# Kernel optimization log

Measured on AMD Instinct MI355X. Metric: run time of the kernel, lower is better.

The kernel has to match this reference:

```python
import jax, jax.numpy as jnp
import numpy as np

B, N, D_IN = 8, 1369, 768
S, D, ITERS = 7, 256, 3
RES, SIGMA = 37, 5.0
EPS = 1e-8


def _ln(x, g, b):
    m = jnp.mean(x, -1, keepdims=True)
    v = jnp.mean((x - m) ** 2, -1, keepdims=True)
    return (x - m) * jax.lax.rsqrt(v + 1e-5) * g + b


def _abs_grid():
    xs = jnp.linspace(-1.0, 1.0, RES)
    ys = jnp.linspace(-1.0, 1.0, RES)
    gx, gy = jnp.meshgrid(xs, ys, indexing='xy')
    return jnp.stack([gx.reshape(-1), gy.reshape(-1)], axis=-1)  # [N,2]


def setup_inputs() -> dict:
    key = jax.random.key(0)
    ks = jax.random.split(key, 40)
    i = iter(range(40))
    def w(shape, scale=0.02):
        return (jax.random.normal(ks[next(i)], shape, jnp.float32) * scale).astype(jnp.float32)
    def zeros(shape):
        return jnp.zeros(shape, jnp.float32)
    xav = float(np.sqrt(6.0 / (S + D)))
    inp = {
        'inputs': jax.random.normal(ks[next(i)], (B, N, D_IN), jnp.float32),
        'slots_init_p': jax.random.uniform(ks[next(i)], (1, S, D), jnp.float32, -xav, xav),
        'S_s0': w((1, S, 1, 2)),
        'S_p0': w((1, S, 1, 2)),
        'im_ln1_g': jnp.ones((D_IN,), jnp.float32), 'im_ln1_b': zeros((D_IN,)),
        'im_w1': w((D_IN, D_IN)), 'im_b1': zeros((D_IN,)),
        'im_w2': w((D_IN, D)), 'im_b2': zeros((D,)),
        'im_ln2_g': jnp.ones((D,), jnp.float32), 'im_ln2_b': zeros((D,)),
        'Wq': w((D, D)), 'Wk': w((D, D)), 'Wv': w((D, D)),
        'g_w': w((2, D)), 'g_b': zeros((D,)),
        'f_w1': w((D, D)), 'f_b1': zeros((D,)),
        'f_w2': w((D, D)), 'f_b2': zeros((D,)),
        'ln_g': jnp.ones((D,), jnp.float32), 'ln_b': zeros((D,)),
        'gru_wih': w((D, 3 * D)), 'gru_whh': w((D, 3 * D)),
        'gru_bih': zeros((3 * D,)), 'gru_bhh': zeros((3 * D,)),
        'mlp_ln_g': jnp.ones((D,), jnp.float32), 'mlp_ln_b': zeros((D,)),
        'mlp_w1': w((D, 4 * D)), 'mlp_b1': zeros((4 * D,)),
        'mlp_w2': w((4 * D, D)), 'mlp_b2': zeros((D,)),
        'fin_w': w((D, D)), 'fin_b': zeros((D,)),
    }
    return inp


def reference(inputs, slots_init_p, S_s0, S_p0,
              im_ln1_g, im_ln1_b, im_w1, im_b1, im_w2, im_b2, im_ln2_g, im_ln2_b,
              Wq, Wk, Wv, g_w, g_b, f_w1, f_b1, f_w2, f_b2,
              ln_g, ln_b, gru_wih, gru_whh, gru_bih, gru_bhh,
              mlp_ln_g, mlp_ln_b, mlp_w1, mlp_b1, mlp_w2, mlp_b2,
              fin_w, fin_b):
    abs_grid = _abs_grid()                    # [N,2], constant buffer
    ag = abs_grid[None, None]                 # [1,1,N,2]
    scale = D ** (-0.5)

    slots = jnp.broadcast_to(slots_init_p, (B, S, D))
    slots_init = slots

    # initial_mlp: LN -> Linear -> ReLU -> Linear -> LN (dropout-free eval path)
    x = _ln(inputs, im_ln1_g, im_ln1_b)
    x = jax.nn.relu(x @ im_w1 + im_b1)
    x = x @ im_w2 + im_b2
    x = _ln(x, im_ln2_g, im_ln2_b)            # [B,N,D]
    KX = x @ Wk                                # slot-independent part of K(inputs)
    VX = x @ Wv

    S_p = jnp.broadcast_to(S_p0, (B, S, 1, 2))
    S_s = jnp.broadcast_to(S_s0, (B, S, 1, 2))

    def f_mlp(z):
        return jax.nn.relu(z @ f_w1 + f_b1) @ f_w2 + f_b2

    attn = None
    slots_prev = slots
    for t in range(ITERS + 1):
        if t == ITERS - 1:  # query_opt straight-through trick
            slots = jax.lax.stop_gradient(slots) + slots_init - jax.lax.stop_gradient(slots_init)
        slots_prev = slots
        sn = _ln(slots, ln_g, ln_b)
        rel = (ag - S_p) / (S_s * SIGMA)      # [B,S,N,2]
        grel = rel @ g_w + g_b                # [B,S,N,D]
        k = f_mlp(KX[:, None] + grel)         # [B,S,N,D]
        v = f_mlp(VX[:, None] + grel)
        q = sn @ Wq                           # [B,S,D]
        dots = jnp.einsum('bsd,bsnd->bsn', q, k) * scale
        attn = jax.nn.softmax(dots, axis=1) + EPS   # softmax over slots
        attn = attn / jnp.sum(attn, -1, keepdims=True)
        updates = jnp.einsum('bsnd,bsn->bsd', v, attn)
        S_p = jnp.einsum('bsn,nd->bsd', attn, abs_grid)[:, :, None, :]
        S_s = jnp.sqrt(jnp.einsum('bsnd,bsn->bsd', (ag - S_p) ** 2, attn))[:, :, None, :]
        if t != ITERS:
            # GRUCell (torch gate order r,z,n)
            gi = updates @ gru_wih + gru_bih
            gh = slots_prev @ gru_whh + gru_bhh
            i_r, i_z, i_n = jnp.split(gi, 3, axis=-1)
            h_r, h_z, h_n = jnp.split(gh, 3, axis=-1)
            r = jax.nn.sigmoid(i_r + h_r)
            z = jax.nn.sigmoid(i_z + h_z)
            n = jnp.tanh(i_n + r * h_n)
            slots = (1.0 - z) * n + z * slots_prev
            # residual pre-norm MLP (dropout identity in eval)
            m = _ln(slots, mlp_ln_g, mlp_ln_b)
            m = jax.nn.relu(m @ mlp_w1 + mlp_b1) @ mlp_w2 + mlp_b2
            slots = slots + m
    out = slots_prev @ fin_w + fin_b
    return out, attn
```

## Files before the change

kernel.cpp:

```cpp
#include <hip/hip_runtime.h>

constexpr int CB   = 8;
constexpr int CN   = 1369;
constexpr int CDIN = 768;
constexpr int CS   = 7;
constexpr int CD   = 256;
constexpr int CITERS = 3;
constexpr int CRES = 37;
constexpr float CSIGMA = 5.0f;
constexpr int CBS = CB * CS;
constexpr int CBN = CB * CN;
constexpr int CKV = 2 * CD;
constexpr float LNEPS = 1e-5f;
constexpr float ATTN_EPS = 1e-8f;

typedef unsigned short u16;
typedef short bs8 __attribute__((ext_vector_type(8)));
typedef float f4 __attribute__((ext_vector_type(4)));

__device__ __forceinline__ float ag_x(int n) { return -1.f + (float)(n % CRES) * (2.f / 36.f); }
__device__ __forceinline__ float ag_y(int n) { return -1.f + (float)(n / CRES) * (2.f / 36.f); }

__device__ __forceinline__ u16 bf_rne(float f) {
    unsigned u = __float_as_uint(f);
    return (u16)((u + 0x7FFFu + ((u >> 16) & 1u)) >> 16);
}
__device__ __forceinline__ float bf_to_f(u16 h) { return __uint_as_float(((unsigned)h) << 16); }

__device__ __forceinline__ void split2b(float v, u16& h, u16& m) {
    h = bf_rne(v);
    m = bf_rne(v - bf_to_f(h));
}

__device__ __forceinline__ void async16(const u16* g, u16* l) {
    __builtin_amdgcn_global_load_lds(
        (const __attribute__((address_space(1))) unsigned int*)g,
        (__attribute__((address_space(3))) unsigned int*)l, 16, 0, 0);
}

__device__ __forceinline__ float block_reduce_sum(float v, float* sbuf) {
    #pragma unroll
    for (int off = 32; off > 0; off >>= 1) v += __shfl_down(v, off, 64);
    if ((threadIdx.x & 63) == 0) sbuf[threadIdx.x >> 6] = v;
    __syncthreads();
    if (threadIdx.x == 0) sbuf[0] = sbuf[0] + sbuf[1] + sbuf[2] + sbuf[3];
    __syncthreads();
    float r = sbuf[0];
    __syncthreads();
    return r;
}

__device__ __forceinline__ float block_reduce_sum128(float v, float* sbuf) {
    #pragma unroll
    for (int off = 32; off > 0; off >>= 1) v += __shfl_down(v, off, 64);
    if ((threadIdx.x & 63) == 0) sbuf[threadIdx.x >> 6] = v;
    __syncthreads();
    float r = sbuf[0] + sbuf[1];
    __syncthreads();
    return r;
}

__global__ __launch_bounds__(256) void ln_planes_kernel(const float* __restrict__ in,
        u16* __restrict__ Yh, u16* __restrict__ Ym,
        const float* __restrict__ g, const float* __restrict__ b, int d) {
    __shared__ float sbuf[8];
    int row = blockIdx.x, t = threadIdx.x;
    const float* x = in + (size_t)row * d;
    float v0 = x[t], v1 = 0.f, v2 = 0.f;
    if (d > 256) { v1 = x[t + 256]; v2 = x[t + 512]; }
    float mean = block_reduce_sum(v0 + v1 + v2, sbuf) / d;
    float d0 = v0 - mean, d1 = v1 - mean, d2 = v2 - mean;
    float pv = (d > 256) ? (d0 * d0 + d1 * d1 + d2 * d2) : (d0 * d0);
    float var = block_reduce_sum(pv, sbuf) / d;
    float rstd = rsqrtf(var + LNEPS);
    {
        float y = d0 * rstd * g[t] + b[t];
        u16 h, m; split2b(y, h, m);
        Yh[(size_t)row * d + t] = h; Ym[(size_t)row * d + t] = m;
    }
    if (d > 256) {
        float y1 = d1 * rstd * g[t + 256] + b[t + 256];
        u16 h, m; split2b(y1, h, m);
        Yh[(size_t)row * d + t + 256] = h; Ym[(size_t)row * d + t + 256] = m;
        float y2 = d2 * rstd * g[t + 512] + b[t + 512];
        split2b(y2, h, m);
        Yh[(size_t)row * d + t + 512] = h; Ym[(size_t)row * d + t + 512] = m;
    }
}

__global__ __launch_bounds__(256) void mega_prep_kernel(
        const float* __restrict__ inputs, u16* __restrict__ xlnh, u16* __restrict__ xlnm,
        const float* __restrict__ im_ln1_g, const float* __restrict__ im_ln1_b,
        const float* __restrict__ im_w1, u16* __restrict__ w1th, u16* __restrict__ w1tm,
        const float* __restrict__ im_w2, u16* __restrict__ w2th, u16* __restrict__ w2tm,
        const float* __restrict__ Wk, const float* __restrict__ Wv,
        const float* __restrict__ Wq,
        const float* __restrict__ f_w1, const float* __restrict__ f_w2,
        u16* __restrict__ kvth, u16* __restrict__ kvtm, float* __restrict__ Pq,
        const float* __restrict__ wih, float* __restrict__ Pg,
        const float* __restrict__ g_w, const float* __restrict__ g_b,
        const float* __restrict__ f_b1,
        float* __restrict__ G2, float* __restrict__ gb1,
        const float* __restrict__ f_b2, const float* __restrict__ bih,
        float* __restrict__ bg, float* __restrict__ wqb) {
    __shared__ float shm[1056];
    int bid = blockIdx.x;
    int t = threadIdx.x;
    if (bid < CBN) {
        int row = bid;
        const float* x = inputs + (size_t)row * CDIN;
        float v0 = x[t], v1 = x[t + 256], v2 = x[t + 512];
        float mean = block_reduce_sum(v0 + v1 + v2, shm) / CDIN;
        float d0 = v0 - mean, d1 = v1 - mean, d2 = v2 - mean;
        float var = block_reduce_sum(d0 * d0 + d1 * d1 + d2 * d2, shm) / CDIN;
        float rstd = rsqrtf(var + LNEPS);
        u16 h, m;
        float y = d0 * rstd * im_ln1_g[t] + im_ln1_b[t];
        split2b(y, h, m);
        xlnh[(size_t)row * CDIN + t] = h; xlnm[(size_t)row * CDIN + t] = m;
        float y1 = d1 * rstd * im_ln1_g[t + 256] + im_ln1_b[t + 256];
        split2b(y1, h, m);
        xlnh[(size_t)row * CDIN + t + 256] = h; xlnm[(size_t)row * CDIN + t + 256] = m;
        float y2 = d2 * rstd * im_ln1_g[t + 512] + im_ln1_b[t + 512];
        split2b(y2, h, m);
        xlnh[(size_t)row * CDIN + t + 512] = h; xlnm[(size_t)row * CDIN + t + 512] = m;
        return;
    }
    if (bid < CBN + 768) {
        int tb = bid - CBN;
        const float* W; u16 *Th, *Tm; int N, bx, by;
        if (tb < 576) { W = im_w1; Th = w1th; Tm = w1tm; N = CDIN; bx = tb % 24; by = tb / 24; }
        else { tb -= 576; W = im_w2; Th = w2th; Tm = w2tm; N = CD; bx = tb % 8; by = tb / 8; }
        int K = CDIN;
        float (*tile)[33] = (float(*)[33])shm;
        int nb = bx * 32, kb = by * 32;
        int tx = t & 31, ty = t >> 5;
        #pragma unroll
        for (int i = 0; i < 32; i += 8)
            tile[ty + i][tx] = W[(size_t)(kb + ty + i) * N + nb + tx];
        __syncthreads();
        #pragma unroll
        for (int i = 0; i < 32; i += 8) {
            float v = tile[tx][ty + i];
            u16 h, m; split2b(v, h, m);
            size_t idx = (size_t)(nb + ty + i) * K + kb + tx;
            Th[idx] = h; Tm[idx] = m;
        }
        return;
    }
    int wb = bid - CBN - 768;
    float* arow = shm;
    int n = t;
    if (wb < 512) {
        const float* A = (wb < 256) ? Wk : Wv;
        int k = wb & 255;
        size_t poff = (wb < 256) ? 0 : (size_t)CD * CD;
        arow[n] = A[k * CD + n];
        __syncthreads();
        float acc = 0.f;
        for (int j = 0; j < CD; j++) acc += arow[j] * f_w1[(size_t)j * CD + n];
        u16 h, m; split2b(acc, h, m);
        kvth[poff + (size_t)n * CD + k] = h;
        kvtm[poff + (size_t)n * CD + k] = m;
    } else if (wb < 768) {
        int k = wb - 512;
        arow[n] = Wq[k * CD + n];
        __syncthreads();
        float acc = 0.f;
        for (int c = 0; c < CD; c++) acc += arow[c] * f_w2[(size_t)n * CD + c];
        Pq[(size_t)k * CD + n] = acc;
    } else if (wb < 1536) {
        int wb2 = wb - 768;
        int k = wb2 & 255;
        int ny = wb2 >> 8;
        arow[n] = f_w2[k * CD + n];
        __syncthreads();
        int nn = ny * 256 + n;
        float acc = 0.f;
        for (int j = 0; j < CD; j++) acc += arow[j] * wih[(size_t)j * (3 * CD) + nn];
        Pg[(size_t)k * (3 * CD) + nn] = acc;
    } else if (wb == 1536) {
        float a0 = 0.f, a1 = 0.f, ab = 0.f;
        for (int j = 0; j < CD; j++) {
            float w = f_w1[j * CD + n];
            a0 += g_w[j] * w;
            a1 += g_w[CD + j] * w;
            ab += g_b[j] * w;
        }
        G2[n] = a0; G2[CD + n] = a1; gb1[n] = ab + f_b1[n];
    } else if (wb <= 1539) {
        int nn = (wb - 1537) * 256 + n;
        float s = bih[nn];
        for (int c = 0; c < CD; c++) s += f_b2[c] * wih[(size_t)c * (3 * CD) + nn];
        bg[nn] = s;
    } else {
        float s = 0.f;
        for (int c = 0; c < CD; c++) s += Wq[n * CD + c] * f_b2[c];
        wqb[n] = s;
    }
}

template<int BN, int NBUF>
__global__ __launch_bounds__(256)
void hgemm2(const u16* __restrict__ Ah, const u16* __restrict__ Am,
            const u16* __restrict__ Bh, const u16* __restrict__ Bm,
            int M, int N, int K, const float* __restrict__ bias, int relu,
            float* __restrict__ Cf, u16* __restrict__ Ch, u16* __restrict__ Cm) {
    constexpr int BP = BN * 32;
    constexpr int SB = 4096 + 2 * BP;
    constexpr int NI = 2 + 2 * (BN / 64);
    constexpr int NF = BN / 32;
    constexpr int PP = BN / 64;
    __shared__ u16 smem[NBUF][SB];
    const int tid = threadIdx.x;

    int bx = blockIdx.x, by = blockIdx.y;
    {
        int gx = gridDim.x;
        int nwg = gx * gridDim.y;
        if (!(nwg & 7)) {
            int bid = by * gx + bx;
            int cpx = nwg >> 3;
            int s = (bid & 7) * cpx + (bid >> 3);
            bx = s % gx; by = s / gx;
        }
    }
    const int m0 = by * 64, n0 = bx * BN;
    const int w = tid >> 6, lane = tid & 63;
    const int wm = w & 1, wn = w >> 1;
    const int l15 = lane & 15, l4 = lane >> 4;

    const u16* srcp[NI];
    int dsto[NI];
    #pragma unroll
    for (int i = 0; i < NI; i++) {
        const u16* bp; int row, r, c;
        if (i < 2) {
            int qq = tid;
            r = qq >> 2;
            c = (qq & 3) ^ ((r ^ (r >> 2)) & 3);
            bp = (i == 0) ? Ah : Am;
            row = m0 + r; row = row < M ? row : M - 1;
            dsto[i] = i * 2048 + w * 512;
        } else {
            int ii = i - 2;
            int plane = ii / PP;
            int sub = ii % PP;
            int qq = sub * 256 + tid;
            r = qq >> 2;
            c = (qq & 3) ^ ((r ^ (r >> 2)) & 3);
            bp = plane ? Bm : Bh;
            row = n0 + r;
            dsto[i] = 4096 + plane * BP + sub * 2048 + w * 512;
        }
        srcp[i] = bp + (size_t)row * K + c * 8;
    }

    f4 acc[2][NF];
    #pragma unroll
    for (int i = 0; i < 2; i++)
        #pragma unroll
        for (int j = 0; j < NF; j++) acc[i][j] = (f4){0.f, 0.f, 0.f, 0.f};

    const int cx8 = (l4 ^ (l15 & 3) ^ ((l15 >> 2) & 3)) * 8;

    const int ns = K / 32;
    #pragma unroll
    for (int d = 0; d < NBUF - 1; d++)
        #pragma unroll
        for (int i = 0; i < NI; i++) async16(srcp[i] + d * 32, &smem[d][dsto[i]]);

    u16* c0 = &smem[0][0];
    u16* c1 = &smem[NBUF > 1 ? 1 : 0][0];
    u16* c2 = &smem[NBUF - 1][0];

    for (int k = 0; k < ns; k++) {
        if constexpr (NBUF == 3) {
            if (k + 2 < ns) {
                #pragma unroll
                for (int i = 0; i < NI; i++) async16(srcp[i] + (k + 2) * 32, c2 + dsto[i]);
                if constexpr (BN == 64) asm volatile("s_waitcnt vmcnt(8)" ::: "memory");
                else                     asm volatile("s_waitcnt vmcnt(12)" ::: "memory");
            } else if (k + 1 < ns) {
                if constexpr (BN == 64) asm volatile("s_waitcnt vmcnt(4)" ::: "memory");
                else                     asm volatile("s_waitcnt vmcnt(6)" ::: "memory");
            } else {
                asm volatile("s_waitcnt vmcnt(0)" ::: "memory");
            }
        } else {
            if (k + 1 < ns) {
                #pragma unroll
                for (int i = 0; i < NI; i++) async16(srcp[i] + (k + 1) * 32, c1 + dsto[i]);
                if constexpr (BN == 64) asm volatile("s_waitcnt vmcnt(4)" ::: "memory");
                else                     asm volatile("s_waitcnt vmcnt(6)" ::: "memory");
            } else {
                asm volatile("s_waitcnt vmcnt(0)" ::: "memory");
            }
        }
        __builtin_amdgcn_s_barrier();
        bs8 ah[2], am[2], bh[NF], bm[NF];
        #pragma unroll
        for (int f = 0; f < 2; f++) {
            int oa = (wm * 32 + f * 16 + l15) * 32 + cx8;
            ah[f] = *(const bs8*)(c0 + oa);
            am[f] = *(const bs8*)(c0 + 2048 + oa);
        }
        #pragma unroll
        for (int f = 0; f < NF; f++) {
            int ob = (wn * (NF * 16) + f * 16 + l15) * 32 + cx8;
            bh[f] = *(const bs8*)(c0 + 4096 + ob);
            bm[f] = *(const bs8*)(c0 + 4096 + BP + ob);
        }
        #pragma unroll
        for (int mf = 0; mf < 2; mf++)
            #pragma unroll
            for (int nf = 0; nf < NF; nf++) {
                acc[mf][nf] = __builtin_amdgcn_mfma_f32_16x16x32_bf16(am[mf], bh[nf], acc[mf][nf], 0, 0, 0);
                acc[mf][nf] = __builtin_amdgcn_mfma_f32_16x16x32_bf16(ah[mf], bm[nf], acc[mf][nf], 0, 0, 0);
                acc[mf][nf] = __builtin_amdgcn_mfma_f32_16x16x32_bf16(ah[mf], bh[nf], acc[mf][nf], 0, 0, 0);
            }
        asm volatile("" ::: "memory");
        __builtin_amdgcn_s_barrier();
        if constexpr (NBUF == 3) { u16* t_ = c0; c0 = c1; c1 = c2; c2 = t_; }
        else                     { u16* t_ = c0; c0 = c1; c1 = t_; }
    }

    #pragma unroll
    for (int mf = 0; mf < 2; mf++)
        #pragma unroll
        for (int i = 0; i < 4; i++) {
            int grow = m0 + wm * 32 + mf * 16 + l4 * 4 + i;
            if (grow < M) {
                #pragma unroll
                for (int nf = 0; nf < NF; nf++) {
                    int col = n0 + wn * (NF * 16) + nf * 16 + l15;
                    float v = acc[mf][nf][i] + (bias ? bias[col] : 0.f);
                    if (relu) v = fmaxf(v, 0.f);
                    if (Cf) Cf[(size_t)grow * N + col] = v;
                    else {
                        u16 h, m; split2b(v, h, m);
                        Ch[(size_t)grow * N + col] = h;
                        Cm[(size_t)grow * N + col] = m;
                    }
                }
            }
        }
}

__global__ __launch_bounds__(128) void rowgemmG_kernel(
        const float* __restrict__ A0, const float* __restrict__ W0,
        const float* __restrict__ b0, float* __restrict__ C0,
        const float* __restrict__ A1, const float* __restrict__ W1,
        const float* __restrict__ b1, float* __restrict__ C1,
        const float* __restrict__ msum, int N, int K) {
    __shared__ float sA[256];
    const float* A = blockIdx.z ? A1 : A0;
    const float* W = blockIdx.z ? W1 : W0;
    const float* B = blockIdx.z ? b1 : b0;
    float* C = blockIdx.z ? C1 : C0;
    int r = blockIdx.x;
    int c = blockIdx.y * 128 + threadIdx.x;
    float scl = blockIdx.z ? 1.f : 1.f / msum[r * 8];
    for (int i = threadIdx.x; i < K; i += 128) sA[i] = A[(size_t)r * K + i] * scl;
    __syncthreads();
    float a0 = 0.f, a1 = 0.f, a2 = 0.f, a3 = 0.f;
    #pragma unroll 4
    for (int k = 0; k < K; k += 4) {
        a0 += sA[k]     * W[(size_t)k * N + c];
        a1 += sA[k + 1] * W[(size_t)(k + 1) * N + c];
        a2 += sA[k + 2] * W[(size_t)(k + 2) * N + c];
        a3 += sA[k + 3] * W[(size_t)(k + 3) * N + c];
    }
    C[(size_t)r * N + c] = (a0 + a1) + (a2 + a3) + B[c];
}

__global__ __launch_bounds__(256) void init_ln_q_kernel(const float* __restrict__ slots_init_p,
        const float* __restrict__ S_s0, const float* __restrict__ S_p0,
        const float* __restrict__ ln_g, const float* __restrict__ ln_b,
        const float* __restrict__ wqb, const float* __restrict__ Pq,
        float* __restrict__ slots, float* __restrict__ S_s, float* __restrict__ S_p,
        float* __restrict__ qwb, float* __restrict__ qb0) {
    __shared__ float sbuf[8];
    __shared__ float sN[CD];
    int row = blockIdx.x, t = threadIdx.x;
    int s = row % CS;
    float x = slots_init_p[s * CD + t];
    slots[row * CD + t] = x;
    if (t < 2) { S_s[row * 2 + t] = S_s0[s * 2 + t]; S_p[row * 2 + t] = S_p0[s * 2 + t]; }
    float mean = block_reduce_sum(x, sbuf) / CD;
    float d0 = x - mean;
    float var = block_reduce_sum(d0 * d0, sbuf) / CD;
    float sn = d0 * rsqrtf(var + LNEPS) * ln_g[t] + ln_b[t];
    sN[t] = sn;
    float qb = block_reduce_sum(sn * wqb[t], sbuf);
    if (t == 0) qb0[row] = qb;
    __syncthreads();
    float acc = 0.f;
    #pragma unroll 4
    for (int k = 0; k < CD; k++) acc += sN[k] * Pq[(size_t)k * CD + t];
    qwb[row * CD + t] = acc;
}

__global__ __launch_bounds__(256) void slotsup_kernel(float* __restrict__ slotsAcc,
        const float* __restrict__ b2, const float* __restrict__ snewb,
        const float* __restrict__ ln_g, const float* __restrict__ ln_b,
        const float* __restrict__ wqb, const float* __restrict__ Pq,
        float* __restrict__ slots, float* __restrict__ qwb, float* __restrict__ qb0) {
    __shared__ float sbuf[8];
    __shared__ float sN[CD];
    int row = blockIdx.x, t = threadIdx.x;
    float v = snewb[row * CD + t] + b2[t] + slotsAcc[row * CD + t];
    slotsAcc[row * CD + t] = 0.f;
    slots[row * CD + t] = v;
    float mean = block_reduce_sum(v, sbuf) / CD;
    float d0 = v - mean;
    float var = block_reduce_sum(d0 * d0, sbuf) / CD;
    float sn = d0 * rsqrtf(var + LNEPS) * ln_g[t] + ln_b[t];
    sN[t] = sn;
    float qb = block_reduce_sum(sn * wqb[t], sbuf);
    if (t == 0) qb0[row] = qb;
    __syncthreads();
    float acc = 0.f;
    #pragma unroll 4
    for (int k = 0; k < CD; k++) acc += sN[k] * Pq[(size_t)k * CD + t];
    qwb[row * CD + t] = acc;
}

__global__ __launch_bounds__(256) void dotsv_kernel(const float* __restrict__ KVX,
        const float* __restrict__ S_p, const float* __restrict__ S_s,
        const float* __restrict__ msum_in, int useMsum,
        const float* __restrict__ G2, const float* __restrict__ gb1,
        const float* __restrict__ qw, const float* __restrict__ qb0,
        float* __restrict__ attn, float* __restrict__ Wacc,
        float* __restrict__ msum_out) {
    __shared__ float sred[4 * CD];
    int b = blockIdx.x;
    int w = threadIdx.x >> 6, l = threadIdx.x & 63;
    int k4 = l * 4;
    float4 g0 = *(const float4*)(G2 + k4);
    float4 g1 = *(const float4*)(G2 + CD + k4);
    float4 gb = *(const float4*)(gb1 + k4);
    float4 qwv[CS]; float px[CS], py[CS], ix[CS], iy[CS], q0[CS];
    #pragma unroll
    for (int s = 0; s < CS; s++) {
        int bs = b * CS + s;
        qwv[s] = *(const float4*)(qw + bs * CD + k4);
        if (useMsum) {
            const float* mp = msum_in + bs * 8;
            float m0 = mp[0];
            float pxv = mp[1] / m0, pyv = mp[2] / m0;
            float sx = sqrtf(fmaxf(mp[3] / m0 - pxv * pxv, 0.f));
            float sy = sqrtf(fmaxf(mp[4] / m0 - pyv * pyv, 0.f));
            px[s] = pxv; py[s] = pyv;
            ix[s] = 1.f / (sx * CSIGMA); iy[s] = 1.f / (sy * CSIGMA);
        } else {
            px[s] = S_p[2 * bs]; py[s] = S_p[2 * bs + 1];
            ix[s] = 1.f / (S_s[2 * bs] * CSIGMA); iy[s] = 1.f / (S_s[2 * bs + 1] * CSIGMA);
        }
        q0[s] = qb0[bs];
    }
    float4 acc[CS];
    #pragma unroll
    for (int s = 0; s < CS; s++) acc[s] = make_float4(0.f, 0.f, 0.f, 0.f);
    float wmv = 0.f;
    int sidx = l / 5;
    int jidx = l - sidx * 5;
    int nbase = blockIdx.y * 16 + w * 4;
    #pragma unroll
    for (int i = 0; i < 4; i++) {
        int n = nbase + i;
        int nc = n < CN ? n : CN - 1;
        const float* rowp = KVX + (size_t)(b * CN + nc) * CKV;
        float4 kx = *(const float4*)(rowp + k4);
        float ax = ag_x(nc), ay = ag_y(nc);
        float dsv[CS];
        #pragma unroll
        for (int s = 0; s < CS; s++) {
            float r0 = (ax - px[s]) * ix[s];
            float r1 = (ay - py[s]) * iy[s];
            float v0 = fmaxf(kx.x + r0 * g0.x + r1 * g1.x + gb.x, 0.f);
            float v1 = fmaxf(kx.y + r0 * g0.y + r1 * g1.y + gb.y, 0.f);
            float v2 = fmaxf(kx.z + r0 * g0.z + r1 * g1.z + gb.z, 0.f);
            float v3 = fmaxf(kx.w + r0 * g0.w + r1 * g1.w + gb.w, 0.f);
            float d = v0 * qwv[s].x + v1 * qwv[s].y + v2 * qwv[s].z + v3 * qwv[s].w;
            #pragma unroll
            for (int off = 32; off > 0; off >>= 1) d += __shfl_xor(d, off, 64);
            dsv[s] = 0.0625f * (d + q0[s]);
        }
        float mx = -1e30f;
        #pragma unroll
        for (int s = 0; s < CS; s++) mx = fmaxf(mx, dsv[s]);
        float sum = 0.f;
        #pragma unroll
        for (int s = 0; s < CS; s++) { dsv[s] = __expf(dsv[s] - mx); sum += dsv[s]; }
        float inv = 1.f / sum;
        #pragma unroll
        for (int s = 0; s < CS; s++) dsv[s] = dsv[s] * inv + ATTN_EPS;
        if (attn && l == 0 && n < CN) {
            #pragma unroll
            for (int s = 0; s < CS; s++)
                attn[(size_t)(b * CS + s) * CN + n] = dsv[s];
        }
        if (msum_out && n < CN) {
            float ax2 = ax * ax, ay2 = ay * ay;
            float a = dsv[0];
            a = (sidx == 1) ? dsv[1] : a;
            a = (sidx == 2) ? dsv[2] : a;
            a = (sidx == 3) ? dsv[3] : a;
            a = (sidx == 4) ? dsv[4] : a;
            a = (sidx == 5) ? dsv[5] : a;
            a = (sidx == 6) ? dsv[6] : a;
            float coef = 1.f;
            coef = (jidx == 1) ? ax : coef;
            coef = (jidx == 2) ? ay : coef;
            coef = (jidx == 3) ? ax2 : coef;
            coef = (jidx == 4) ? ay2 : coef;
            wmv += a * coef;
        }
        if (Wacc && n < CN) {
            float4 vx = *(const float4*)(rowp + CD + k4);
            #pragma unroll
            for (int s = 0; s < CS; s++) {
                float r0 = (ax - px[s]) * ix[s];
                float r1 = (ay - py[s]) * iy[s];
                float a = dsv[s];
                acc[s].x += a * fmaxf(vx.x + r0 * g0.x + r1 * g1.x + gb.x, 0.f);
                acc[s].y += a * fmaxf(vx.y + r0 * g0.y + r1 * g1.y + gb.y, 0.f);
                acc[s].z += a * fmaxf(vx.z + r0 * g0.z + r1 * g1.z + gb.z, 0.f);
                acc[s].w += a * fmaxf(vx.w + r0 * g0.w + r1 * g1.w + gb.w, 0.f);
            }
        }
    }
    if (Wacc) {
        for (int s = 0; s < CS; s++) {
            ((float4*)sred)[w * 64 + l] = acc[s];
            __syncthreads();
            if (threadIdx.x < CD) {
                float v = sred[threadIdx.x] + sred[CD + threadIdx.x]
                        + sred[2 * CD + threadIdx.x] + sred[3 * CD + threadIdx.x];
                atomicAdd(&Wacc[(size_t)(b * CS + s) * CD + threadIdx.x], v);
            }
            __syncthreads();
        }
    }
    if (msum_out) {
        if (l < 35) sred[w * 35 + l] = wmv;
        __syncthreads();
        if (threadIdx.x < 35) {
            float v = sred[threadIdx.x] + sred[35 + threadIdx.x]
                    + sred[70 + threadIdx.x] + sred[105 + threadIdx.x];
            int s = threadIdx.x / 5, j = threadIdx.x % 5;
            atomicAdd(&msum_out[(size_t)(b * CS + s) * 8 + j], v);
        }
    }
}

__global__ __launch_bounds__(128) void gate_mlp1_kernel(const float* __restrict__ giRaw,
        const float* __restrict__ ghRaw, const float* __restrict__ slots,
        const float* __restrict__ mg, const float* __restrict__ mb,
        const float* __restrict__ mlp_w1, const float* __restrict__ mlp_b1,
        const float* __restrict__ w2,
        float* __restrict__ snewb, float* __restrict__ slotsAcc,
        float* __restrict__ WaccZ, float* __restrict__ msumZ) {
    __shared__ float sbuf[4];
    __shared__ float sM[CD];
    __shared__ float sH1[128];
    int row = blockIdx.x, t = threadIdx.x;
    float snew[2];
    #pragma unroll
    for (int e = 0; e < 2; e++) {
        int tt = t + e * 128;
        float gi0 = giRaw[row * 3 * CD + tt];
        float gi1 = giRaw[row * 3 * CD + CD + tt];
        float gi2 = giRaw[row * 3 * CD + 2 * CD + tt];
        float gh0 = ghRaw[row * 3 * CD + tt];
        float gh1 = ghRaw[row * 3 * CD + CD + tt];
        float gh2 = ghRaw[row * 3 * CD + 2 * CD + tt];
        float r = 1.f / (1.f + expf(-(gi0 + gh0)));
        float z = 1.f / (1.f + expf(-(gi1 + gh1)));
        float nn = tanhf(gi2 + r * gh2);
        snew[e] = (1.f - z) * nn + z * slots[row * CD + tt];
    }
    if (blockIdx.y == 0) {
        snewb[row * CD + t] = snew[0];
        snewb[row * CD + t + 128] = snew[1];
        WaccZ[row * CD + t] = 0.f;
        WaccZ[row * CD + t + 128] = 0.f;
        if (t < 8) msumZ[row * 8 + t] = 0.f;
    }
    float mean = block_reduce_sum128(snew[0] + snew[1], sbuf) / CD;
    float d0 = snew[0] - mean, d1 = snew[1] - mean;
    float var = block_reduce_sum128(d0 * d0 + d1 * d1, sbuf) / CD;
    float rstd = rsqrtf(var + LNEPS);
    sM[t]       = d0 * rstd * mg[t] + mb[t];
    sM[t + 128] = d1 * rstd * mg[t + 128] + mb[t + 128];
    __syncthreads();
    int c = blockIdx.y * 128 + t;
    float a0 = 0.f, a1 = 0.f, a2 = 0.f, a3 = 0.f;
    #pragma unroll 4
    for (int k = 0; k < CD; k += 4) {
        a0 += sM[k]     * mlp_w1[(size_t)k * (4 * CD) + c];
        a1 += sM[k + 1] * mlp_w1[(size_t)(k + 1) * (4 * CD) + c];
        a2 += sM[k + 2] * mlp_w1[(size_t)(k + 2) * (4 * CD) + c];
        a3 += sM[k + 3] * mlp_w1[(size_t)(k + 3) * (4 * CD) + c];
    }
    sH1[t] = fmaxf((a0 + a1) + (a2 + a3) + mlp_b1[c], 0.f);
    __syncthreads();
    float p0 = 0.f, p1 = 0.f;
    const float* w2b = w2 + (size_t)blockIdx.y * 128 * CD;
    #pragma unroll 4
    for (int cc = 0; cc < 128; cc++) {
        float h = sH1[cc];
        p0 += h * w2b[(size_t)cc * CD + t];
        p1 += h * w2b[(size_t)cc * CD + t + 128];
    }
    atomicAdd(&slotsAcc[row * CD + t], p0);
    atomicAdd(&slotsAcc[row * CD + t + 128], p1);
}

__global__ __launch_bounds__(128) void final_kernel(const float* __restrict__ slots,
        const float* __restrict__ fin_w, const float* __restrict__ fin_b,
        float* __restrict__ out0, float* __restrict__ attn,
        const float* __restrict__ msum) {
    int row = blockIdx.x;
    if (blockIdx.y == 2) {
        float inv = 1.f / msum[(size_t)row * 8];
        float* up = attn + (size_t)row * CN;
        for (int n = threadIdx.x; n < CN; n += 128) up[n] *= inv;
        return;
    }
    __shared__ float sA[CD];
    for (int i = threadIdx.x; i < CD; i += 128) sA[i] = slots[(size_t)row * CD + i];
    __syncthreads();
    int c = blockIdx.y * 128 + threadIdx.x;
    float a0 = 0.f, a1 = 0.f, a2 = 0.f, a3 = 0.f;
    #pragma unroll 4
    for (int k = 0; k < CD; k += 4) {
        a0 += sA[k]     * fin_w[(size_t)k * CD + c];
        a1 += sA[k + 1] * fin_w[(size_t)(k + 1) * CD + c];
        a2 += sA[k + 2] * fin_w[(size_t)(k + 2) * CD + c];
        a3 += sA[k + 3] * fin_w[(size_t)(k + 3) * CD + c];
    }
    out0[(size_t)row * CD + c] = (a0 + a1) + (a2 + a3) + fin_b[c];
}

extern "C" void kernel_launch(void* const* d_in, const int* in_sizes, int n_in,
                              void* d_out, int out_size, void* d_ws, size_t ws_size,
                              hipStream_t stream) {
    (void)in_sizes; (void)n_in; (void)out_size;
    const float* inputs       = (const float*)d_in[0];
    const float* slots_init_p = (const float*)d_in[1];
    const float* S_s0         = (const float*)d_in[2];
    const float* S_p0         = (const float*)d_in[3];
    const float* im_ln1_g = (const float*)d_in[4];
    const float* im_ln1_b = (const float*)d_in[5];
    const float* im_w1    = (const float*)d_in[6];
    const float* im_b1    = (const float*)d_in[7];
    const float* im_w2    = (const float*)d_in[8];
    const float* im_b2    = (const float*)d_in[9];
    const float* im_ln2_g = (const float*)d_in[10];
    const float* im_ln2_b = (const float*)d_in[11];
    const float* Wq  = (const float*)d_in[12];
    const float* Wk  = (const float*)d_in[13];
    const float* Wv  = (const float*)d_in[14];
    const float* g_w = (const float*)d_in[15];
    const float* g_b = (const float*)d_in[16];
    const float* f_w1 = (const float*)d_in[17];
    const float* f_b1 = (const float*)d_in[18];
    const float* f_w2 = (const float*)d_in[19];
    const float* f_b2 = (const float*)d_in[20];
    const float* ln_g = (const float*)d_in[21];
    const float* ln_b = (const float*)d_in[22];
    const float* gru_wih = (const float*)d_in[23];
    const float* gru_whh = (const float*)d_in[24];
    const float* gru_bih = (const float*)d_in[25];
    const float* gru_bhh = (const float*)d_in[26];
    const float* mlp_ln_g = (const float*)d_in[27];
    const float* mlp_ln_b = (const float*)d_in[28];
    const float* mlp_w1 = (const float*)d_in[29];
    const float* mlp_b1 = (const float*)d_in[30];
    const float* mlp_w2 = (const float*)d_in[31];
    const float* mlp_b2 = (const float*)d_in[32];
    const float* fin_w = (const float*)d_in[33];
    const float* fin_b = (const float*)d_in[34];

    char* base = (char*)d_ws;
    size_t off = 0;
    auto take = [&](size_t bytes) { void* p = base + off; off += (bytes + 255) & ~(size_t)255; return p; };

    float* R1 = (float*)take((size_t)CBN * CDIN * 4);
    float* R2 = (float*)take((size_t)CBN * CDIN * 4);
    u16* w1th = (u16*)take((size_t)CDIN * CDIN * 2);
    u16* w1tm = (u16*)take((size_t)CDIN * CDIN * 2);
    u16* w2th = (u16*)take((size_t)CDIN * CD * 2);
    u16* w2tm = (u16*)take((size_t)CDIN * CD * 2);
    u16* kvth = (u16*)take((size_t)CKV * CD * 2);
    u16* kvtm = (u16*)take((size_t)CKV * CD * 2);
    float* G2b  = (float*)take((size_t)2 * CD * 4);
    float* gb1b = (float*)take((size_t)CD * 4);
    float* Pq   = (float*)take((size_t)CD * CD * 4);
    float* Pg   = (float*)take((size_t)CD * 3 * CD * 4);
    float* bgv  = (float*)take((size_t)3 * CD * 4);
    float* wqbb = (float*)take((size_t)CD * 4);
    float* qwb   = (float*)take((size_t)CBS * CD * 4);
    float* qb0b  = (float*)take((size_t)CBS * 4);
    float* Wacc  = (float*)take(((size_t)CBS * CD * 2 + 2 * CBS * 8) * 4);
    float* msumA = Wacc + (size_t)CBS * CD;
    float* msumB = msumA + (size_t)CBS * 8;
    float* slotsAcc = msumB + (size_t)CBS * 8;
    float* giRaw = (float*)take((size_t)CBS * 3 * CD * 4);
    float* ghRaw = (float*)take((size_t)CBS * 3 * CD * 4);
    float* snewb = (float*)take((size_t)CBS * CD * 4);
    float* S_pB  = (float*)take((size_t)CBS * 2 * 4);
    float* S_sB  = (float*)take((size_t)CBS * 2 * 4);
    float* slots = (float*)take((size_t)CBS * CD * 4);
    if (ws_size < off) return;

    float* msum[2] = {msumA, msumB};

    u16* xlnh = (u16*)R1;
    u16* xlnm = xlnh + (size_t)CBN * CDIN;
    u16* X1h  = (u16*)R2;
    u16* X1m  = X1h + (size_t)CBN * CDIN;
    float* xD = R1;
    u16* xDnh = (u16*)(R1 + (size_t)CBN * CD);
    u16* xDnm = xDnh + (size_t)CBN * CD;
    float* KVX = R2;

    float* out0 = (float*)d_out;
    float* attnb = out0 + CBS * CD;

    dim3 blk(256);
    const int gM = (CBN + 63) / 64;
    dim3 gridBN(CB, 86);

    mega_prep_kernel<<<dim3(CBN + 768 + 1541), blk, 0, stream>>>(
        inputs, xlnh, xlnm, im_ln1_g, im_ln1_b,
        im_w1, w1th, w1tm, im_w2, w2th, w2tm,
        Wk, Wv, Wq, f_w1, f_w2, kvth, kvtm, Pq,
        gru_wih, Pg, g_w, g_b, f_b1, G2b, gb1b,
        f_b2, gru_bih, bgv, wqbb);
    hipMemsetAsync(Wacc, 0, ((size_t)CBS * CD * 2 + 2 * CBS * 8) * sizeof(float), stream);

    hgemm2<128,2><<<dim3(CDIN/128, gM), blk, 0, stream>>>(xlnh, xlnm, w1th, w1tm,
        CBN, CDIN, CDIN, im_b1, 1, nullptr, X1h, X1m);
    hgemm2<64,3><<<dim3(CD/64, gM), blk, 0, stream>>>(X1h, X1m, w2th, w2tm,
        CBN, CD, CDIN, im_b2, 0, xD, nullptr, nullptr);
    ln_planes_kernel<<<CBN, blk, 0, stream>>>(xD, xDnh, xDnm, im_ln2_g, im_ln2_b, CD);
    hgemm2<128,2><<<dim3(CKV/128, gM), blk, 0, stream>>>(xDnh, xDnm, kvth, kvtm,
        CBN, CKV, CD, nullptr, 0, KVX, nullptr, nullptr);
    init_ln_q_kernel<<<CBS, blk, 0, stream>>>(slots_init_p, S_s0, S_p0,
        ln_g, ln_b, wqbb, Pq, slots, S_sB, S_pB, qwb, qb0b);

    for (int t = 0; t < CITERS; t++) {
        dotsv_kernel<<<gridBN, blk, 0, stream>>>(KVX, S_pB, S_sB,
            msum[(t + 1) & 1], t > 0 ? 1 : 0, G2b, gb1b,
            qwb, qb0b, nullptr, Wacc, msum[t & 1]);
        rowgemmG_kernel<<<dim3(CBS, 3*CD/128, 2), dim3(128), 0, stream>>>(
            Wacc, Pg, bgv, giRaw, slots, gru_whh, gru_bhh, ghRaw, msum[t & 1], 3 * CD, CD);
        gate_mlp1_kernel<<<dim3(CBS, 8), dim3(128), 0, stream>>>(giRaw, ghRaw, slots,
            mlp_ln_g, mlp_ln_b, mlp_w1, mlp_b1, mlp_w2, snewb, slotsAcc,
            Wacc, msum[(t + 1) & 1]);
        slotsup_kernel<<<CBS, blk, 0, stream>>>(slotsAcc, mlp_b2, snewb,
            ln_g, ln_b, wqbb, Pq, slots, qwb, qb0b);
    }
    dotsv_kernel<<<gridBN, blk, 0, stream>>>(KVX, S_pB, S_sB,
        msum[0], 1, G2b, gb1b, qwb, qb0b, attnb, nullptr, msum[1]);
    final_kernel<<<dim3(CBS, 3), dim3(128), 0, stream>>>(slots, fin_w, fin_b,
        out0, attnb, msum[1]);
}
```

Measured before the change: 562.4 us.

## Split-K the second input MLP GEMM and fold memset into prep kernel

The 768->256 GEMM (only 4 column tiles wide) now runs with a K-split of two via gridDim.z, writing two fp32 partial outputs that the LayerNorm kernel sums together with the bias before normalizing. This doubles the number of workgroups for a narrow GEMM to improve CU occupancy, at the cost of an extra partial-output write and read. Separately, the hipMemsetAsync of the accumulator buffer is replaced by extra zeroing blocks appended to the mega prep kernel, removing one launch. The LN kernel is specialized to D=256.

```diff
diff --git a/kernel.cpp b/kernel.cpp
--- a/kernel.cpp
+++ b/kernel.cpp
@@ -60,32 +60,22 @@
     return r;
 }
 
-__global__ __launch_bounds__(256) void ln_planes_kernel(const float* __restrict__ in,
+__global__ __launch_bounds__(256) void ln_planes_sum2_kernel(
+        const float* __restrict__ xa, const float* __restrict__ xb,
+        const float* __restrict__ bias,
         u16* __restrict__ Yh, u16* __restrict__ Ym,
-        const float* __restrict__ g, const float* __restrict__ b, int d) {
+        const float* __restrict__ g, const float* __restrict__ b) {
     __shared__ float sbuf[8];
     int row = blockIdx.x, t = threadIdx.x;
-    const float* x = in + (size_t)row * d;
-    float v0 = x[t], v1 = 0.f, v2 = 0.f;
-    if (d > 256) { v1 = x[t + 256]; v2 = x[t + 512]; }
-    float mean = block_reduce_sum(v0 + v1 + v2, sbuf) / d;
-    float d0 = v0 - mean, d1 = v1 - mean, d2 = v2 - mean;
-    float pv = (d > 256) ? (d0 * d0 + d1 * d1 + d2 * d2) : (d0 * d0);
-    float var = block_reduce_sum(pv, sbuf) / d;
+    size_t idx = (size_t)row * CD + t;
+    float v0 = xa[idx] + xb[idx] + bias[t];
+    float mean = block_reduce_sum(v0, sbuf) / CD;
+    float d0 = v0 - mean;
+    float var = block_reduce_sum(d0 * d0, sbuf) / CD;
     float rstd = rsqrtf(var + LNEPS);
-    {
-        float y = d0 * rstd * g[t] + b[t];
-        u16 h, m; split2b(y, h, m);
-        Yh[(size_t)row * d + t] = h; Ym[(size_t)row * d + t] = m;
-    }
-    if (d > 256) {
-        float y1 = d1 * rstd * g[t + 256] + b[t + 256];
-        u16 h, m; split2b(y1, h, m);
-        Yh[(size_t)row * d + t + 256] = h; Ym[(size_t)row * d + t + 256] = m;
-        float y2 = d2 * rstd * g[t + 512] + b[t + 512];
-        split2b(y2, h, m);
-        Yh[(size_t)row * d + t + 512] = h; Ym[(size_t)row * d + t + 512] = m;
-    }
+    float y = d0 * rstd * g[t] + b[t];
+    u16 h, m; split2b(y, h, m);
+    Yh[idx] = h; Ym[idx] = m;
 }
 
 __global__ __launch_bounds__(256) void mega_prep_kernel(
@@ -102,7 +92,8 @@
         const float* __restrict__ f_b1,
         float* __restrict__ G2, float* __restrict__ gb1,
         const float* __restrict__ f_b2, const float* __restrict__ bih,
-        float* __restrict__ bg, float* __restrict__ wqb) {
+        float* __restrict__ bg, float* __restrict__ wqb,
+        float* __restrict__ accZ, int accN) {
     __shared__ float shm[1056];
     int bid = blockIdx.x;
     int t = threadIdx.x;
@@ -146,6 +137,13 @@
             size_t idx = (size_t)(nb + ty + i) * K + kb + tx;
             Th[idx] = h; Tm[idx] = m;
         }
+        return;
+    }
+    if (bid >= CBN + 768 + 1541) {
+        int zb = bid - (CBN + 768 + 1541);
+        int fi = (zb * 256 + t) * 4;
+        if (fi + 3 < accN) *(f4*)(accZ + fi) = (f4){0.f, 0.f, 0.f, 0.f};
+        else for (int i = fi; i < accN; i++) accZ[i] = 0.f;
         return;
     }
     int wb = bid - CBN - 768;
@@ -205,7 +203,8 @@
 void hgemm2(const u16* __restrict__ Ah, const u16* __restrict__ Am,
             const u16* __restrict__ Bh, const u16* __restrict__ Bm,
             int M, int N, int K, const float* __restrict__ bias, int relu,
-            float* __restrict__ Cf, u16* __restrict__ Ch, u16* __restrict__ Cm) {
+            float* __restrict__ Cf, u16* __restrict__ Ch, u16* __restrict__ Cm,
+            float* __restrict__ Cf2) {
     constexpr int BP = BN * 32;
     constexpr int SB = 4096 + 2 * BP;
     constexpr int NI = 2 + 2 * (BN / 64);
@@ -225,6 +224,9 @@
             bx = s % gx; by = s / gx;
         }
     }
+    const int Keff = K / (int)gridDim.z;
+    const int koff = (int)blockIdx.z * Keff;
+    float* Cout = (blockIdx.z == 0) ? Cf : Cf2;
     const int m0 = by * 64, n0 = bx * BN;
     const int w = tid >> 6, lane = tid & 63;
     const int wm = w & 1, wn = w >> 1;
@@ -253,7 +255,7 @@
             row = n0 + r;
             dsto[i] = 4096 + plane * BP + sub * 2048 + w * 512;
         }
-        srcp[i] = bp + (size_t)row * K + c * 8;
+        srcp[i] = bp + (size_t)row * K + koff + c * 8;
     }
 
     f4 acc[2][NF];
@@ -264,7 +266,7 @@
 
     const int cx8 = (l4 ^ (l15 & 3) ^ ((l15 >> 2) & 3)) * 8;
 
-    const int ns = K / 32;
+    const int ns = Keff / 32;
     #pragma unroll
     for (int d = 0; d < NBUF - 1; d++)
         #pragma unroll
@@ -336,7 +338,7 @@
                     int col = n0 + wn * (NF * 16) + nf * 16 + l15;
                     float v = acc[mf][nf][i] + (bias ? bias[col] : 0.f);
                     if (relu) v = fmaxf(v, 0.f);
-                    if (Cf) Cf[(size_t)grow * N + col] = v;
+                    if (Cout) Cout[(size_t)grow * N + col] = v;
                     else {
                         u16 h, m; split2b(v, h, m);
                         Ch[(size_t)grow * N + col] = h;
@@ -704,7 +706,8 @@
     float* wqbb = (float*)take((size_t)CD * 4);
     float* qwb   = (float*)take((size_t)CBS * CD * 4);
     float* qb0b  = (float*)take((size_t)CBS * 4);
-    float* Wacc  = (float*)take(((size_t)CBS * CD * 2 + 2 * CBS * 8) * 4);
+    const int ACCN = CBS * CD * 2 + 2 * CBS * 8;
+    float* Wacc  = (float*)take((size_t)ACCN * 4);
     float* msumA = Wacc + (size_t)CBS * CD;
     float* msumB = msumA + (size_t)CBS * 8;
     float* slotsAcc = msumB + (size_t)CBS * 8;
@@ -722,8 +725,9 @@
     u16* xlnm = xlnh + (size_t)CBN * CDIN;
     u16* X1h  = (u16*)R2;
     u16* X1m  = X1h + (size_t)CBN * CDIN;
-    float* xD = R1;
-    u16* xDnh = (u16*)(R1 + (size_t)CBN * CD);
+    float* xDa = R1;
+    float* xDb = R1 + (size_t)CBN * CD;
+    u16* xDnh = (u16*)(R1 + (size_t)2 * CBN * CD);
     u16* xDnm = xDnh + (size_t)CBN * CD;
     float* KVX = R2;
 
@@ -733,22 +737,23 @@
     dim3 blk(256);
     const int gM = (CBN + 63) / 64;
     dim3 gridBN(CB, 86);
-
-    mega_prep_kernel<<<dim3(CBN + 768 + 1541), blk, 0, stream>>>(
+    const int ZBLK = (ACCN + 1023) / 1024;
+
+    mega_prep_kernel<<<dim3(CBN + 768 + 1541 + ZBLK), blk, 0, stream>>>(
         inputs, xlnh, xlnm, im_ln1_g, im_ln1_b,
         im_w1, w1th, w1tm, im_w2, w2th, w2tm,
         Wk, Wv, Wq, f_w1, f_w2, kvth, kvtm, Pq,
         gru_wih, Pg, g_w, g_b, f_b1, G2b, gb1b,
-        f_b2, gru_bih, bgv, wqbb);
-    hipMemsetAsync(Wacc, 0, ((size_t)CBS * CD * 2 + 2 * CBS * 8) * sizeof(float), stream);
+        f_b2, gru_bih, bgv, wqbb, Wacc, ACCN);
 
     hgemm2<128,2><<<dim3(CDIN/128, gM), blk, 0, stream>>>(xlnh, xlnm, w1th, w1tm,
-        CBN, CDIN, CDIN, im_b1, 1, nullptr, X1h, X1m);
-    hgemm2<64,3><<<dim3(CD/64, gM), blk, 0, stream>>>(X1h, X1m, w2th, w2tm,
-        CBN, CD, CDIN, im_b2, 0, xD, nullptr, nullptr);
-    ln_planes_kernel<<<CBN, blk, 0, stream>>>(xD, xDnh, xDnm, im_ln2_g, im_ln2_b, CD);
+        CBN, CDIN, CDIN, im_b1, 1, nullptr, X1h, X1m, nullptr);
+    hgemm2<64,3><<<dim3(CD/64, gM, 2), blk, 0, stream>>>(X1h, X1m, w2th, w2tm,
+        CBN, CD, CDIN, nullptr, 0, xDa, nullptr, nullptr, xDb);
+    ln_planes_sum2_kernel<<<CBN, blk, 0, stream>>>(xDa, xDb, im_b2,
+        xDnh, xDnm, im_ln2_g, im_ln2_b);
     hgemm2<128,2><<<dim3(CKV/128, gM), blk, 0, stream>>>(xDnh, xDnm, kvth, kvtm,
-        CBN, CKV, CD, nullptr, 0, KVX, nullptr, nullptr);
+        CBN, CKV, CD, nullptr, 0, KVX, nullptr, nullptr, nullptr);
     init_ln_q_kernel<<<CBS, blk, 0, stream>>>(slots_init_p, S_s0, S_p0,
         ln_g, ln_b, wqbb, Pq, slots, S_sB, S_pB, qwb, qb0b);
 
```

Result: no change. 568.9 us (+1.2%).
